# Optimization experiments

Hardware: AMD Instinct MI355X
Metric: run time of the kernel (lower is better)

## Reference

```python
import jax, jax.numpy as jnp
import numpy as np

WIN = (2, 7, 7)
DIL = (1, 2, 2)
SHIFT = (1, 3, 3)
HEADS = 3

def _rel_index(win):
    # relative position index, identical to the torch buffer construction
    cs = np.stack(np.meshgrid(np.arange(win[0]), np.arange(win[1]), np.arange(win[2]), indexing='ij'))
    flat = cs.reshape(3, -1)                                  # (3, N)
    rel = (flat[:, :, None] - flat[:, None, :]).transpose(1, 2, 0)  # (N, N, 3)
    rel[..., 0] += win[0] - 1
    rel[..., 1] += win[1] - 1
    rel[..., 2] += win[2] - 1
    rel[..., 1] *= 2 * win[2] - 1
    rel[..., 0] *= (2 * win[1] - 1) * (2 * win[2] - 1)
    return rel.sum(-1)                                        # (N, N) int

REL_IDX = _rel_index(WIN)

def _partition(x, win, dil):
    # x: (B, S, H, W, C) -> (numWin*B, N, C) with dilated window layout
    B, S, H, W, C = x.shape
    x = x.reshape(B, S // (dil[0] * win[0]), dil[0], win[0],
                  H // (dil[1] * win[1]), dil[1], win[1],
                  W // (dil[2] * win[2]), dil[2], win[2], C)
    x = x.transpose(0, 2, 5, 8, 1, 4, 7, 3, 6, 9, 10)
    return x.reshape(-1, win[0] * win[1] * win[2], C)

def _reverse(wins, win, dil, S, H, W, C):
    B = wins.shape[0] * win[0] * win[1] * win[2] // (S * H * W)
    x = wins.reshape(B, dil[0], dil[1], dil[2],
                     S // (dil[0] * win[0]), H // (dil[1] * win[1]), W // (dil[2] * win[2]),
                     win[0], win[1], win[2], C)
    x = x.transpose(0, 4, 1, 7, 5, 2, 8, 6, 3, 9, 10)
    return x.reshape(B, S, H, W, C)

def setup_inputs() -> dict:
    key = jax.random.key(0)
    ks = jax.random.split(key, 4)
    B, S, H, W, C = 4, 8, 112, 112, 96
    tbl = (2 * WIN[0] - 1) * (2 * WIN[1] - 1) * (2 * WIN[2] - 1)
    return {
        'x': jax.random.normal(ks[0], (B, S * H * W, C), jnp.float32),
        'qkv_w': jax.random.normal(ks[1], (3 * C, C), jnp.float32) * 0.02,
        'qkv_b': jnp.zeros((3 * C,), jnp.float32),
        'proj_w': jax.random.normal(ks[2], (C, C), jnp.float32) * 0.02,
        'proj_b': jnp.zeros((C,), jnp.float32),
        'rel_bias_table': jax.random.normal(ks[3], (tbl, HEADS), jnp.float32) * 0.02,
        'S': 8, 'H': 112, 'W': 112,
    }

def reference(x, qkv_w, qkv_b, proj_w, proj_b, rel_bias_table, S, H, W):
    B, L, C = x.shape
    hd = C // HEADS
    scale = hd ** -0.5
    x = x.reshape(B, S, H, W, C)
    true = tuple(w * d for w, d in zip(WIN, DIL))
    tshift = tuple(s * d for s, d in zip(SHIFT, DIL))
    pad_d = (-S) % true[0]; pad_b = (-H) % true[1]; pad_r = (-W) % true[2]
    x = jnp.pad(x, ((0, 0), (0, pad_d), (0, pad_b), (0, pad_r), (0, 0)))
    Sp, Hp, Wp = S + pad_d, H + pad_b, W + pad_r
    if any(s > 0 for s in SHIFT):
        x = jnp.roll(x, (-tshift[0], -tshift[1], -tshift[2]), axis=(1, 2, 3))
    xw = _partition(x, WIN, DIL)                              # (B_, N, C)
    B_, N, _ = xw.shape
    qkv = (xw @ qkv_w.T + qkv_b).reshape(B_, N, 3, HEADS, hd).transpose(2, 0, 3, 1, 4)
    q, k, v = qkv[0] * scale, qkv[1], qkv[2]                  # (B_, h, N, d)
    attn = jnp.einsum('bhnd,bhmd->bhnm', q, k)
    bias = rel_bias_table[REL_IDX.reshape(-1)].reshape(N, N, HEADS).transpose(2, 0, 1)
    attn = jax.nn.softmax(attn + bias[None], axis=-1)
    out = jnp.einsum('bhnm,bhmd->bhnd', attn, v).transpose(0, 2, 1, 3).reshape(B_, N, C)
    out = out @ proj_w.T + proj_b
    x = _reverse(out, WIN, DIL, Sp, Hp, Wp, C)
    if any(s > 0 for s in SHIFT):
        x = jnp.roll(x, tshift, axis=(1, 2, 3))
    x = x[:, :S, :H, :W, :]
    return x.reshape(B, S * H * W, C)
```

## Files before the change

kernel.cpp:

```cpp
#include <hip/hip_runtime.h>
#include <hip/hip_bf16.h>


typedef __attribute__((ext_vector_type(8))) short short8;
typedef __attribute__((ext_vector_type(4))) float f32x4;

#define WQ_ELEMS (288 * 96)
#define WP_ELEMS (96 * 96)
#define BIAS_ELEMS (3 * 112 * 112)
#define LOG2E 1.4426950408889634f

__device__ __forceinline__ unsigned short f2bf(float f) {
  __hip_bfloat16 h = __float2bfloat16(f);
  return *reinterpret_cast<unsigned short*>(&h);
}

__device__ __forceinline__ unsigned int pack_bf2(float a, float b) {
  unsigned int r;
  asm("v_cvt_pk_bf16_f32 %0, %1, %2" : "=v"(r) : "v"(a), "v"(b));
  return r;
}

__global__ __launch_bounds__(256) void prep_kernel(
    const float* __restrict__ qkv_w, const float* __restrict__ proj_w,
    const float* __restrict__ tbl, unsigned short* __restrict__ wq,
    unsigned short* __restrict__ wp, float* __restrict__ bias) {
  int i = blockIdx.x * 256 + threadIdx.x;
  if (i < WQ_ELEMS) wq[i] = f2bf(qkv_w[i]);
  if (i < WP_ELEMS) wp[i] = f2bf(proj_w[i]);
  if (i < BIAS_ELEMS) {
    int h = i / 12544; int rem = i - h * 12544;
    int m = rem / 112; int n = rem - m * 112;
    float v = -1e30f;
    if (m < 98 && n < 98) {
      int m0 = m / 49, mr = m - m0 * 49, m1 = mr / 7, m2 = mr - m1 * 7;
      int n0 = n / 49, nr = n - n0 * 49, n1 = nr / 7, n2 = nr - n1 * 7;
      int idx = (m0 - n0 + 1) * 169 + (m1 - n1 + 6) * 13 + (m2 - n2 + 6);
      v = tbl[idx * 3 + h] * LOG2E;
    }
    bias[i] = v;
  }
}


__global__ __launch_bounds__(256) void winattn_kernel(
    const float* __restrict__ x, const float* __restrict__ qkv_b,
    const float* __restrict__ proj_b, const unsigned short* __restrict__ wq,
    const unsigned short* __restrict__ wp, const float* __restrict__ bias,
    float* __restrict__ out) {

  __shared__ __align__(16) unsigned short lds[40512];
  __shared__ int eoff[98];

  unsigned short* Qf  = lds;
  unsigned short* Kf  = lds + 9408;
  unsigned short* Vtf = lds + 18816;
  unsigned short* Xf  = lds + 31104;

  const int tid  = threadIdx.x;
  const int wv   = tid >> 6;
  const int lane = tid & 63;
  const int l    = lane & 15;
  const int q    = lane >> 4;

  const short8 zero8 = {0, 0, 0, 0, 0, 0, 0, 0};

  int t1 = blockIdx.x;
  const int wb = t1 & 7;  t1 >>= 3;
  const int hb = t1 & 7;  t1 >>= 3;
  const int sb = t1 & 3;  t1 >>= 2;
  const int d2 = t1 & 1;  t1 >>= 1;
  const int d1 = t1 & 1;  t1 >>= 1;
  const int b  = t1;

  for (int i = tid; i < 768; i += 256)
    reinterpret_cast<unsigned*>(Vtf + 10752)[i] = 0;
  if (tid < 98) {
    int wi0 = tid / 49; int r = tid - wi0 * 49;
    int wi1 = r / 7;    int wi2 = r - wi1 * 7;
    int s  = sb * 2 + wi0;            int so = (s + 1) & 7;
    int hh = (hb * 2 + d1) * 7 + wi1; int ho = hh + 6; if (ho >= 112) ho -= 112;
    int ww = (wb * 2 + d2) * 7 + wi2; int wo = ww + 6; if (wo >= 112) wo -= 112;
    eoff[tid] = (b * 100352 + (so * 112 + ho) * 112 + wo) * 96;
  }
  __syncthreads();

  for (int i = tid; i < 2352; i += 256) {
    int row = i / 24, c4 = i - row * 24;
    float4 v = *reinterpret_cast<const float4*>(x + eoff[row] + c4 * 4);
    uint2 u;
    u.x = pack_bf2(v.x, v.y); u.y = pack_bf2(v.z, v.w);
    *reinterpret_cast<uint2*>(&Xf[((c4 >> 1) * 98 + row) * 8 + (c4 & 1) * 4]) = u;
  }
  __syncthreads();

  const float qscale = 0.17677669529663687f * LOG2E;
  for (int ct = wv; ct < 12; ct += 4) {
    int mch = ct * 16 + l;
    short8 a0 = *reinterpret_cast<const short8*>(wq + mch * 96 +      q * 8);
    short8 a1 = *reinterpret_cast<const short8*>(wq + mch * 96 + 32 + q * 8);
    short8 a2 = *reinterpret_cast<const short8*>(wq + mch * 96 + 64 + q * 8);
    float4 bv = *reinterpret_cast<const float4*>(qkv_b + ct * 16 + q * 4);
    bool isQ = (ct < 6);
    float sc = isQ ? qscale : 1.0f;
    unsigned short* dst = isQ ? Qf : Kf;
    int c0 = (isQ ? ct * 16 : (ct - 6) * 16) + q * 4;
    unsigned short* const dstp = &dst[(c0 >> 3) * 784 + (c0 & 7)];
#pragma unroll
    for (int tt = 0; tt < 7; tt++) {
      int tok = tt * 16 + l;
      short8 b0 = zero8, b1 = zero8, b2 = zero8;
      if (tok < 98) {
        b0 = *reinterpret_cast<const short8*>(&Xf[(( q    ) * 98 + tok) * 8]);
        b1 = *reinterpret_cast<const short8*>(&Xf[((4 + q ) * 98 + tok) * 8]);
        b2 = *reinterpret_cast<const short8*>(&Xf[((8 + q ) * 98 + tok) * 8]);
      }
      f32x4 acc = {0.f, 0.f, 0.f, 0.f};
      acc = __builtin_amdgcn_mfma_f32_16x16x32_bf16(a0, b0, acc, 0, 0, 0);
      acc = __builtin_amdgcn_mfma_f32_16x16x32_bf16(a1, b1, acc, 0, 0, 0);
      acc = __builtin_amdgcn_mfma_f32_16x16x32_bf16(a2, b2, acc, 0, 0, 0);
      uint2 pk;
      pk.x = pack_bf2((acc[0] + bv.x) * sc, (acc[1] + bv.y) * sc);
      pk.y = pack_bf2((acc[2] + bv.z) * sc, (acc[3] + bv.w) * sc);
      if (tok < 98)
        *reinterpret_cast<uint2*>(&dstp[tok * 8]) = pk;
    }
  }

  for (int mt = wv; mt < 7; mt += 4) {
    int tokf = mt * 16 + l;
    short8 a0 = zero8, a1 = zero8, a2 = zero8;
    if (tokf < 98) {
      a0 = *reinterpret_cast<const short8*>(&Xf[(( q    ) * 98 + tokf) * 8]);
      a1 = *reinterpret_cast<const short8*>(&Xf[((4 + q ) * 98 + tokf) * 8]);
      a2 = *reinterpret_cast<const short8*>(&Xf[((8 + q ) * 98 + tokf) * 8]);
    }
    int tok0 = mt * 16 + q * 4;
#pragma unroll
    for (int vt = 0; vt < 6; vt++) {
      int ch = vt * 16 + l;
      short8 b0 = *reinterpret_cast<const short8*>(wq + (192 + ch) * 96 +      q * 8);
      short8 b1 = *reinterpret_cast<const short8*>(wq + (192 + ch) * 96 + 32 + q * 8);
      short8 b2 = *reinterpret_cast<const short8*>(wq + (192 + ch) * 96 + 64 + q * 8);
      f32x4 acc = {0.f, 0.f, 0.f, 0.f};
      acc = __builtin_amdgcn_mfma_f32_16x16x32_bf16(a0, b0, acc, 0, 0, 0);
      acc = __builtin_amdgcn_mfma_f32_16x16x32_bf16(a1, b1, acc, 0, 0, 0);
      acc = __builtin_amdgcn_mfma_f32_16x16x32_bf16(a2, b2, acc, 0, 0, 0);
      float bvv = qkv_b[192 + ch];
      uint2 pk;
      pk.x = pack_bf2(acc[0] + bvv, acc[1] + bvv);
      pk.y = pack_bf2(acc[2] + bvv, acc[3] + bvv);
      *reinterpret_cast<uint2*>(&Vtf[((tok0 >> 3) * 96 + ch) * 8 + (tok0 & 7)]) = pk;
    }
  }
  __syncthreads();

  unsigned short* PwW = Xf + wv * 2048;
  const int pbase = ((q >> 1) * 16 + l) * 8 + (q & 1) * 4;
  const int rbase = (q * 16 + l) * 8;
  {
    uint2 z; z.x = 0; z.y = 0;
    *reinterpret_cast<uint2*>(&PwW[1792 + lane * 4]) = z;
  }
  for (int p = wv; p < 21; p += 4) {
    int h = p / 7, mt = p - h * 7;
    int qtok = mt * 16 + l;
    short8 qa = zero8;
    if (qtok < 98)
      qa = *reinterpret_cast<const short8*>(&Qf[((h * 4 + q) * 98 + qtok) * 8]);
    f32x4 s[7];
#pragma unroll
    for (int nt = 0; nt < 7; nt++) {
      int key = nt * 16 + l;
      short8 kb = zero8;
      if (key < 98)
        kb = *reinterpret_cast<const short8*>(&Kf[((h * 4 + q) * 98 + key) * 8]);
      f32x4 z = {0.f, 0.f, 0.f, 0.f};
      s[nt] = __builtin_amdgcn_mfma_f32_16x16x32_bf16(kb, qa, z, 0, 0, 0);
    }
    const float* bh = bias + h * 12544 + qtok * 112 + q * 4;
#pragma unroll
    for (int nt = 0; nt < 7; nt++) {
      float4 bv = *reinterpret_cast<const float4*>(bh + nt * 16);
      s[nt][0] += bv.x; s[nt][1] += bv.y; s[nt][2] += bv.z; s[nt][3] += bv.w;
    }
    float m[7];
#pragma unroll
    for (int nt = 0; nt < 7; nt++)
      m[nt] = fmaxf(fmaxf(s[nt][0], s[nt][1]), fmaxf(s[nt][2], s[nt][3]));
    float mx = fmaxf(fmaxf(fmaxf(m[0], m[1]), fmaxf(m[2], m[3])),
                     fmaxf(fmaxf(m[4], m[5]), m[6]));
    mx = fmaxf(mx, __shfl_xor(mx, 16));
    mx = fmaxf(mx, __shfl_xor(mx, 32));
    float t[7];
#pragma unroll
    for (int nt = 0; nt < 7; nt++) {
      float e0 = exp2f(s[nt][0] - mx);
      float e1 = exp2f(s[nt][1] - mx);
      float e2 = exp2f(s[nt][2] - mx);
      float e3 = exp2f(s[nt][3] - mx);
      s[nt][0] = e0; s[nt][1] = e1; s[nt][2] = e2; s[nt][3] = e3;
      t[nt] = (e0 + e1) + (e2 + e3);
    }
    float sum = ((t[0] + t[1]) + (t[2] + t[3])) + ((t[4] + t[5]) + t[6]);
    sum += __shfl_xor(sum, 16);
    sum += __shfl_xor(sum, 32);
    float inv = __builtin_amdgcn_rcpf(sum);
#pragma unroll
    for (int nt = 0; nt < 7; nt++) {
      uint2 pk;
      pk.x = pack_bf2(s[nt][0], s[nt][1]);
      pk.y = pack_bf2(s[nt][2], s[nt][3]);
      *reinterpret_cast<uint2*>(&PwW[pbase + nt * 256]) = pk;
    }
    asm volatile("s_waitcnt lgkmcnt(0)" ::: "memory");
    f32x4 o0 = {0.f, 0.f, 0.f, 0.f}, o1 = {0.f, 0.f, 0.f, 0.f};
#pragma unroll
    for (int kt = 0; kt < 4; kt++) {
      short8 pa = *reinterpret_cast<const short8*>(&PwW[rbase + kt * 512]);
      short8 v0 = *reinterpret_cast<const short8*>(&Vtf[((kt * 4 + q) * 96 + h * 32 + l) * 8]);
      short8 v1 = *reinterpret_cast<const short8*>(&Vtf[((kt * 4 + q) * 96 + h * 32 + 16 + l) * 8]);
      o0 = __builtin_amdgcn_mfma_f32_16x16x32_bf16(v0, pa, o0, 0, 0, 0);
      o1 = __builtin_amdgcn_mfma_f32_16x16x32_bf16(v1, pa, o1, 0, 0, 0);
    }
    if (qtok < 98) {
      int c0 = h * 32 + q * 4;
      uint2 pk0;
      pk0.x = pack_bf2(o0[0] * inv, o0[1] * inv);
      pk0.y = pack_bf2(o0[2] * inv, o0[3] * inv);
      *reinterpret_cast<uint2*>(&Qf[((c0 >> 3) * 98 + qtok) * 8 + (c0 & 7)]) = pk0;
      int c1 = c0 + 16;
      uint2 pk1;
      pk1.x = pack_bf2(o1[0] * inv, o1[1] * inv);
      pk1.y = pack_bf2(o1[2] * inv, o1[3] * inv);
      *reinterpret_cast<uint2*>(&Qf[((c1 >> 3) * 98 + qtok) * 8 + (c1 & 7)]) = pk1;
    }
  }
  __syncthreads();

  for (int tt = wv; tt < 7; tt += 4) {
    int tok = tt * 16 + l;
    short8 b0 = zero8, b1 = zero8, b2 = zero8;
    if (tok < 98) {
      b0 = *reinterpret_cast<const short8*>(&Qf[(( q    ) * 98 + tok) * 8]);
      b1 = *reinterpret_cast<const short8*>(&Qf[((4 + q ) * 98 + tok) * 8]);
      b2 = *reinterpret_cast<const short8*>(&Qf[((8 + q ) * 98 + tok) * 8]);
    }
    int off = eoff[(tok < 98) ? tok : 0];
#pragma unroll
    for (int ct = 0; ct < 6; ct++) {
      int mch = ct * 16 + l;
      short8 a0 = *reinterpret_cast<const short8*>(wp + mch * 96 +      q * 8);
      short8 a1 = *reinterpret_cast<const short8*>(wp + mch * 96 + 32 + q * 8);
      short8 a2 = *reinterpret_cast<const short8*>(wp + mch * 96 + 64 + q * 8);
      f32x4 acc = {0.f, 0.f, 0.f, 0.f};
      acc = __builtin_amdgcn_mfma_f32_16x16x32_bf16(a0, b0, acc, 0, 0, 0);
      acc = __builtin_amdgcn_mfma_f32_16x16x32_bf16(a1, b1, acc, 0, 0, 0);
      acc = __builtin_amdgcn_mfma_f32_16x16x32_bf16(a2, b2, acc, 0, 0, 0);
      float4 pb = *reinterpret_cast<const float4*>(proj_b + ct * 16 + q * 4);
      if (tok < 98) {
        float4 o;
        o.x = acc[0] + pb.x; o.y = acc[1] + pb.y;
        o.z = acc[2] + pb.z; o.w = acc[3] + pb.w;
        *reinterpret_cast<float4*>(out + off + ct * 16 + q * 4) = o;
      }
    }
  }
}

extern "C" void kernel_launch(void* const* d_in, const int* in_sizes, int n_in,
                              void* d_out, int out_size, void* d_ws, size_t ws_size,
                              hipStream_t stream) {
  const float* x      = (const float*)d_in[0];
  const float* qkv_w  = (const float*)d_in[1];
  const float* qkv_b  = (const float*)d_in[2];
  const float* proj_w = (const float*)d_in[3];
  const float* proj_b = (const float*)d_in[4];
  const float* tbl    = (const float*)d_in[5];

  unsigned short* wq = (unsigned short*)d_ws;
  unsigned short* wp = wq + WQ_ELEMS;
  float* bias = (float*)((char*)d_ws + (WQ_ELEMS + WP_ELEMS) * 2);

  prep_kernel<<<(BIAS_ELEMS + 255) / 256, 256, 0, stream>>>(qkv_w, proj_w, tbl,
                                                            wq, wp, bias);
  winattn_kernel<<<4096, 256, 0, stream>>>(x, qkv_b, proj_b, wq, wp, bias,
                                           (float*)d_out);
}
```

Measured before the change: 458.4 us.

## Software-pipeline attention tiles with double-buffered scores and hardware exp

Splits the per-tile attention into stages (QK MFMA with bias prefetch, softmax, P store, PV MFMA) and interleaves consecutive tiles in a double-buffered, manually unrolled schedule. Global bias loads and QK MFMAs for the next tile can then overlap the softmax and PV of the current one. Also replaces exp2f with the raw v_exp_f32 instruction and removes an explicit LDS wait. In exchange, register pressure roughly doubles for the score buffers, which may cut occupancy or cause spills.

```diff
diff --git a/kernel.cpp b/kernel.cpp
--- a/kernel.cpp
+++ b/kernel.cpp
@@ -18,6 +18,12 @@
 __device__ __forceinline__ unsigned int pack_bf2(float a, float b) {
   unsigned int r;
   asm("v_cvt_pk_bf16_f32 %0, %1, %2" : "=v"(r) : "v"(a), "v"(b));
+  return r;
+}
+
+__device__ __forceinline__ float exp2_hw(float x) {
+  float r;
+  asm("v_exp_f32 %0, %1" : "=v"(r) : "v"(x));
   return r;
 }
 
@@ -162,13 +168,17 @@
     uint2 z; z.x = 0; z.y = 0;
     *reinterpret_cast<uint2*>(&PwW[1792 + lane * 4]) = z;
   }
-  for (int p = wv; p < 21; p += 4) {
-    int h = p / 7, mt = p - h * 7;
-    int qtok = mt * 16 + l;
+
+  auto Af = [&](int p, f32x4* s, float4* bvv, int& qtok, int& h) {
+    h = p / 7; int mt = p - h * 7;
+    qtok = mt * 16 + l;
+    const float* bh = bias + h * 12544 + qtok * 112 + q * 4;
+#pragma unroll
+    for (int nt = 0; nt < 7; nt++)
+      bvv[nt] = *reinterpret_cast<const float4*>(bh + nt * 16);
     short8 qa = zero8;
     if (qtok < 98)
       qa = *reinterpret_cast<const short8*>(&Qf[((h * 4 + q) * 98 + qtok) * 8]);
-    f32x4 s[7];
 #pragma unroll
     for (int nt = 0; nt < 7; nt++) {
       int key = nt * 16 + l;
@@ -178,42 +188,47 @@
       f32x4 z = {0.f, 0.f, 0.f, 0.f};
       s[nt] = __builtin_amdgcn_mfma_f32_16x16x32_bf16(kb, qa, z, 0, 0, 0);
     }
-    const float* bh = bias + h * 12544 + qtok * 112 + q * 4;
+  };
+
+  auto Bf = [&](f32x4* s, const float4* bvv, uint2* pk, float& inv) {
 #pragma unroll
     for (int nt = 0; nt < 7; nt++) {
-      float4 bv = *reinterpret_cast<const float4*>(bh + nt * 16);
-      s[nt][0] += bv.x; s[nt][1] += bv.y; s[nt][2] += bv.z; s[nt][3] += bv.w;
+      s[nt][0] += bvv[nt].x; s[nt][1] += bvv[nt].y;
+      s[nt][2] += bvv[nt].z; s[nt][3] += bvv[nt].w;
     }
     float m[7];
 #pragma unroll
     for (int nt = 0; nt < 7; nt++)
       m[nt] = fmaxf(fmaxf(s[nt][0], s[nt][1]), fmaxf(s[nt][2], s[nt][3]));
-    float mx = fmaxf(fmaxf(fmaxf(m[0], m[1]), fmaxf(m[2], m[3])),
-                     fmaxf(fmaxf(m[4], m[5]), m[6]));
+    float ma = fmaxf(fmaxf(m[0], m[1]), m[2]);
+    float mb = fmaxf(fmaxf(m[3], m[4]), m[5]);
+    float mx = fmaxf(fmaxf(ma, mb), m[6]);
     mx = fmaxf(mx, __shfl_xor(mx, 16));
     mx = fmaxf(mx, __shfl_xor(mx, 32));
     float t[7];
 #pragma unroll
     for (int nt = 0; nt < 7; nt++) {
-      float e0 = exp2f(s[nt][0] - mx);
-      float e1 = exp2f(s[nt][1] - mx);
-      float e2 = exp2f(s[nt][2] - mx);
-      float e3 = exp2f(s[nt][3] - mx);
-      s[nt][0] = e0; s[nt][1] = e1; s[nt][2] = e2; s[nt][3] = e3;
+      float e0 = exp2_hw(s[nt][0] - mx);
+      float e1 = exp2_hw(s[nt][1] - mx);
+      float e2 = exp2_hw(s[nt][2] - mx);
+      float e3 = exp2_hw(s[nt][3] - mx);
       t[nt] = (e0 + e1) + (e2 + e3);
+      pk[nt].x = pack_bf2(e0, e1);
+      pk[nt].y = pack_bf2(e2, e3);
     }
     float sum = ((t[0] + t[1]) + (t[2] + t[3])) + ((t[4] + t[5]) + t[6]);
     sum += __shfl_xor(sum, 16);
     sum += __shfl_xor(sum, 32);
-    float inv = __builtin_amdgcn_rcpf(sum);
-#pragma unroll
-    for (int nt = 0; nt < 7; nt++) {
-      uint2 pk;
-      pk.x = pack_bf2(s[nt][0], s[nt][1]);
-      pk.y = pack_bf2(s[nt][2], s[nt][3]);
-      *reinterpret_cast<uint2*>(&PwW[pbase + nt * 256]) = pk;
-    }
-    asm volatile("s_waitcnt lgkmcnt(0)" ::: "memory");
+    inv = __builtin_amdgcn_rcpf(sum);
+  };
+
+  auto Cf = [&](const uint2* pk) {
+#pragma unroll
+    for (int nt = 0; nt < 7; nt++)
+      *reinterpret_cast<uint2*>(&PwW[pbase + nt * 256]) = pk[nt];
+  };
+
+  auto DEf = [&](int h, int qtok, float inv) {
     f32x4 o0 = {0.f, 0.f, 0.f, 0.f}, o1 = {0.f, 0.f, 0.f, 0.f};
 #pragma unroll
     for (int kt = 0; kt < 4; kt++) {
@@ -235,6 +250,44 @@
       pk1.y = pack_bf2(o1[2] * inv, o1[3] * inv);
       *reinterpret_cast<uint2*>(&Qf[((c1 >> 3) * 98 + qtok) * 8 + (c1 & 7)]) = pk1;
     }
+  };
+
+  f32x4 sA[7], sB[7];
+  float4 bvA[7], bvB[7];
+  uint2 pkA[7], pkB[7];
+  float ivA, ivB;
+  int hA, hB, qtA, qtB;
+
+  Af(wv, sA, bvA, qtA, hA);
+  Bf(sA, bvA, pkA, ivA);
+
+  Cf(pkA);
+  Af(wv + 4, sB, bvB, qtB, hB);
+  DEf(hA, qtA, ivA);
+  Bf(sB, bvB, pkB, ivB);
+
+  Cf(pkB);
+  Af(wv + 8, sA, bvA, qtA, hA);
+  DEf(hB, qtB, ivB);
+  Bf(sA, bvA, pkA, ivA);
+
+  Cf(pkA);
+  Af(wv + 12, sB, bvB, qtB, hB);
+  DEf(hA, qtA, ivA);
+  Bf(sB, bvB, pkB, ivB);
+
+  Cf(pkB);
+  Af(wv + 16, sA, bvA, qtA, hA);
+  DEf(hB, qtB, ivB);
+  Bf(sA, bvA, pkA, ivA);
+
+  Cf(pkA);
+  if (wv == 0) Af(20, sB, bvB, qtB, hB);
+  DEf(hA, qtA, ivA);
+  if (wv == 0) {
+    Bf(sB, bvB, pkB, ivB);
+    Cf(pkB);
+    DEf(hB, qtB, ivB);
   }
   __syncthreads();
 
```

Measured after the change: 442.2 us. 1.04x faster.

## Double block to 512 threads and rebalance per-window work across eight waves

Applied to the files above, without the earlier changes.

Launches 512-thread blocks (8 waves) per window and redistributes the QKV, attention, and projection work across them. Q/K and V projection tiles now share one loop, and the output projection is split into 42 independent tiles. To fit eight waves in the shared scratch, each wave's P buffer is halved and the PV product is done in two passes. The bias is preloaded as the MFMA accumulator, and exp2 uses the raw v_exp_f32 instruction. This trades more waves per window, and so more latency hiding, for tighter LDS reuse, which needs an added zero-write, and slightly lower exp accuracy.

```diff
diff --git a/kernel.cpp b/kernel.cpp
--- a/kernel.cpp
+++ b/kernel.cpp
@@ -18,6 +18,12 @@
 __device__ __forceinline__ unsigned int pack_bf2(float a, float b) {
   unsigned int r;
   asm("v_cvt_pk_bf16_f32 %0, %1, %2" : "=v"(r) : "v"(a), "v"(b));
+  return r;
+}
+
+__device__ __forceinline__ float exp2_hw(float x) {
+  float r;
+  asm("v_exp_f32 %0, %1" : "=v"(r) : "v"(x));
   return r;
 }
 
@@ -43,7 +49,7 @@
 }
 
 
-__global__ __launch_bounds__(256) void winattn_kernel(
+__global__ __launch_bounds__(512, 4) void winattn_kernel(
     const float* __restrict__ x, const float* __restrict__ qkv_b,
     const float* __restrict__ proj_b, const unsigned short* __restrict__ wq,
     const unsigned short* __restrict__ wp, const float* __restrict__ bias,
@@ -73,7 +79,7 @@
   const int d1 = t1 & 1;  t1 >>= 1;
   const int b  = t1;
 
-  for (int i = tid; i < 768; i += 256)
+  for (int i = tid; i < 768; i += 512)
     reinterpret_cast<unsigned*>(Vtf + 10752)[i] = 0;
   if (tid < 98) {
     int wi0 = tid / 49; int r = tid - wi0 * 49;
@@ -85,7 +91,7 @@
   }
   __syncthreads();
 
-  for (int i = tid; i < 2352; i += 256) {
+  for (int i = tid; i < 2352; i += 512) {
     int row = i / 24, c4 = i - row * 24;
     float4 v = *reinterpret_cast<const float4*>(x + eoff[row] + c4 * 4);
     uint2 u;
@@ -95,129 +101,142 @@
   __syncthreads();
 
   const float qscale = 0.17677669529663687f * LOG2E;
-  for (int ct = wv; ct < 12; ct += 4) {
-    int mch = ct * 16 + l;
-    short8 a0 = *reinterpret_cast<const short8*>(wq + mch * 96 +      q * 8);
-    short8 a1 = *reinterpret_cast<const short8*>(wq + mch * 96 + 32 + q * 8);
-    short8 a2 = *reinterpret_cast<const short8*>(wq + mch * 96 + 64 + q * 8);
-    float4 bv = *reinterpret_cast<const float4*>(qkv_b + ct * 16 + q * 4);
-    bool isQ = (ct < 6);
-    float sc = isQ ? qscale : 1.0f;
-    unsigned short* dst = isQ ? Qf : Kf;
-    int c0 = (isQ ? ct * 16 : (ct - 6) * 16) + q * 4;
-    unsigned short* const dstp = &dst[(c0 >> 3) * 784 + (c0 & 7)];
-#pragma unroll
-    for (int tt = 0; tt < 7; tt++) {
-      int tok = tt * 16 + l;
-      short8 b0 = zero8, b1 = zero8, b2 = zero8;
-      if (tok < 98) {
-        b0 = *reinterpret_cast<const short8*>(&Xf[(( q    ) * 98 + tok) * 8]);
-        b1 = *reinterpret_cast<const short8*>(&Xf[((4 + q ) * 98 + tok) * 8]);
-        b2 = *reinterpret_cast<const short8*>(&Xf[((8 + q ) * 98 + tok) * 8]);
+  for (int j = wv; j < 19; j += 8) {
+    if (j < 12) {
+      int ct = j;
+      int mch = ct * 16 + l;
+      short8 a0 = *reinterpret_cast<const short8*>(wq + mch * 96 +      q * 8);
+      short8 a1 = *reinterpret_cast<const short8*>(wq + mch * 96 + 32 + q * 8);
+      short8 a2 = *reinterpret_cast<const short8*>(wq + mch * 96 + 64 + q * 8);
+      float4 bv = *reinterpret_cast<const float4*>(qkv_b + ct * 16 + q * 4);
+      bool isQ = (ct < 6);
+      float sc = isQ ? qscale : 1.0f;
+      unsigned short* dst = isQ ? Qf : Kf;
+      int c0 = (isQ ? ct * 16 : (ct - 6) * 16) + q * 4;
+      unsigned short* const dstp = &dst[(c0 >> 3) * 784 + (c0 & 7)];
+#pragma unroll
+      for (int tt = 0; tt < 7; tt++) {
+        int tok = tt * 16 + l;
+        short8 b0 = zero8, b1 = zero8, b2 = zero8;
+        if (tok < 98) {
+          b0 = *reinterpret_cast<const short8*>(&Xf[(( q    ) * 98 + tok) * 8]);
+          b1 = *reinterpret_cast<const short8*>(&Xf[((4 + q ) * 98 + tok) * 8]);
+          b2 = *reinterpret_cast<const short8*>(&Xf[((8 + q ) * 98 + tok) * 8]);
+        }
+        f32x4 acc = {0.f, 0.f, 0.f, 0.f};
+        acc = __builtin_amdgcn_mfma_f32_16x16x32_bf16(a0, b0, acc, 0, 0, 0);
+        acc = __builtin_amdgcn_mfma_f32_16x16x32_bf16(a1, b1, acc, 0, 0, 0);
+        acc = __builtin_amdgcn_mfma_f32_16x16x32_bf16(a2, b2, acc, 0, 0, 0);
+        uint2 pk;
+        pk.x = pack_bf2((acc[0] + bv.x) * sc, (acc[1] + bv.y) * sc);
+        pk.y = pack_bf2((acc[2] + bv.z) * sc, (acc[3] + bv.w) * sc);
+        if (tok < 98)
+          *reinterpret_cast<uint2*>(&dstp[tok * 8]) = pk;
       }
-      f32x4 acc = {0.f, 0.f, 0.f, 0.f};
-      acc = __builtin_amdgcn_mfma_f32_16x16x32_bf16(a0, b0, acc, 0, 0, 0);
-      acc = __builtin_amdgcn_mfma_f32_16x16x32_bf16(a1, b1, acc, 0, 0, 0);
-      acc = __builtin_amdgcn_mfma_f32_16x16x32_bf16(a2, b2, acc, 0, 0, 0);
-      uint2 pk;
-      pk.x = pack_bf2((acc[0] + bv.x) * sc, (acc[1] + bv.y) * sc);
-      pk.y = pack_bf2((acc[2] + bv.z) * sc, (acc[3] + bv.w) * sc);
-      if (tok < 98)
-        *reinterpret_cast<uint2*>(&dstp[tok * 8]) = pk;
-    }
-  }
-
-  for (int mt = wv; mt < 7; mt += 4) {
-    int tokf = mt * 16 + l;
-    short8 a0 = zero8, a1 = zero8, a2 = zero8;
-    if (tokf < 98) {
-      a0 = *reinterpret_cast<const short8*>(&Xf[(( q    ) * 98 + tokf) * 8]);
-      a1 = *reinterpret_cast<const short8*>(&Xf[((4 + q ) * 98 + tokf) * 8]);
-      a2 = *reinterpret_cast<const short8*>(&Xf[((8 + q ) * 98 + tokf) * 8]);
-    }
-    int tok0 = mt * 16 + q * 4;
-#pragma unroll
-    for (int vt = 0; vt < 6; vt++) {
-      int ch = vt * 16 + l;
-      short8 b0 = *reinterpret_cast<const short8*>(wq + (192 + ch) * 96 +      q * 8);
-      short8 b1 = *reinterpret_cast<const short8*>(wq + (192 + ch) * 96 + 32 + q * 8);
-      short8 b2 = *reinterpret_cast<const short8*>(wq + (192 + ch) * 96 + 64 + q * 8);
-      f32x4 acc = {0.f, 0.f, 0.f, 0.f};
-      acc = __builtin_amdgcn_mfma_f32_16x16x32_bf16(a0, b0, acc, 0, 0, 0);
-      acc = __builtin_amdgcn_mfma_f32_16x16x32_bf16(a1, b1, acc, 0, 0, 0);
-      acc = __builtin_amdgcn_mfma_f32_16x16x32_bf16(a2, b2, acc, 0, 0, 0);
-      float bvv = qkv_b[192 + ch];
-      uint2 pk;
-      pk.x = pack_bf2(acc[0] + bvv, acc[1] + bvv);
-      pk.y = pack_bf2(acc[2] + bvv, acc[3] + bvv);
-      *reinterpret_cast<uint2*>(&Vtf[((tok0 >> 3) * 96 + ch) * 8 + (tok0 & 7)]) = pk;
+    } else {
+      int mt = j - 12;
+      int tokf = mt * 16 + l;
+      short8 a0 = zero8, a1 = zero8, a2 = zero8;
+      if (tokf < 98) {
+        a0 = *reinterpret_cast<const short8*>(&Xf[(( q    ) * 98 + tokf) * 8]);
+        a1 = *reinterpret_cast<const short8*>(&Xf[((4 + q ) * 98 + tokf) * 8]);
+        a2 = *reinterpret_cast<const short8*>(&Xf[((8 + q ) * 98 + tokf) * 8]);
+      }
+      int tok0 = mt * 16 + q * 4;
+#pragma unroll
+      for (int vt = 0; vt < 6; vt++) {
+        int ch = vt * 16 + l;
+        short8 b0 = *reinterpret_cast<const short8*>(wq + (192 + ch) * 96 +      q * 8);
+        short8 b1 = *reinterpret_cast<const short8*>(wq + (192 + ch) * 96 + 32 + q * 8);
+        short8 b2 = *reinterpret_cast<const short8*>(wq + (192 + ch) * 96 + 64 + q * 8);
+        f32x4 acc = {0.f, 0.f, 0.f, 0.f};
+        acc = __builtin_amdgcn_mfma_f32_16x16x32_bf16(a0, b0, acc, 0, 0, 0);
+        acc = __builtin_amdgcn_mfma_f32_16x16x32_bf16(a1, b1, acc, 0, 0, 0);
+        acc = __builtin_amdgcn_mfma_f32_16x16x32_bf16(a2, b2, acc, 0, 0, 0);
+        float bvv = qkv_b[192 + ch];
+        uint2 pk;
+        pk.x = pack_bf2(acc[0] + bvv, acc[1] + bvv);
+        pk.y = pack_bf2(acc[2] + bvv, acc[3] + bvv);
+        *reinterpret_cast<uint2*>(&Vtf[((tok0 >> 3) * 96 + ch) * 8 + (tok0 & 7)]) = pk;
+      }
     }
   }
   __syncthreads();
 
-  unsigned short* PwW = Xf + wv * 2048;
+  unsigned short* PwW = Xf + wv * 1024;
   const int pbase = ((q >> 1) * 16 + l) * 8 + (q & 1) * 4;
   const int rbase = (q * 16 + l) * 8;
-  {
-    uint2 z; z.x = 0; z.y = 0;
-    *reinterpret_cast<uint2*>(&PwW[1792 + lane * 4]) = z;
-  }
-  for (int p = wv; p < 21; p += 4) {
+
+  for (int p = wv; p < 21; p += 8) {
     int h = p / 7, mt = p - h * 7;
     int qtok = mt * 16 + l;
+    const float* bh = bias + h * 12544 + qtok * 112 + q * 4;
+    f32x4 s[7];
+#pragma unroll
+    for (int nt = 0; nt < 7; nt++) {
+      float4 bv = *reinterpret_cast<const float4*>(bh + nt * 16);
+      f32x4 a = {bv.x, bv.y, bv.z, bv.w};
+      s[nt] = a;
+    }
     short8 qa = zero8;
     if (qtok < 98)
       qa = *reinterpret_cast<const short8*>(&Qf[((h * 4 + q) * 98 + qtok) * 8]);
-    f32x4 s[7];
 #pragma unroll
     for (int nt = 0; nt < 7; nt++) {
       int key = nt * 16 + l;
       short8 kb = zero8;
       if (key < 98)
         kb = *reinterpret_cast<const short8*>(&Kf[((h * 4 + q) * 98 + key) * 8]);
-      f32x4 z = {0.f, 0.f, 0.f, 0.f};
-      s[nt] = __builtin_amdgcn_mfma_f32_16x16x32_bf16(kb, qa, z, 0, 0, 0);
-    }
-    const float* bh = bias + h * 12544 + qtok * 112 + q * 4;
-#pragma unroll
-    for (int nt = 0; nt < 7; nt++) {
-      float4 bv = *reinterpret_cast<const float4*>(bh + nt * 16);
-      s[nt][0] += bv.x; s[nt][1] += bv.y; s[nt][2] += bv.z; s[nt][3] += bv.w;
+      s[nt] = __builtin_amdgcn_mfma_f32_16x16x32_bf16(kb, qa, s[nt], 0, 0, 0);
     }
     float m[7];
 #pragma unroll
     for (int nt = 0; nt < 7; nt++)
       m[nt] = fmaxf(fmaxf(s[nt][0], s[nt][1]), fmaxf(s[nt][2], s[nt][3]));
-    float mx = fmaxf(fmaxf(fmaxf(m[0], m[1]), fmaxf(m[2], m[3])),
-                     fmaxf(fmaxf(m[4], m[5]), m[6]));
+    float ma = fmaxf(fmaxf(m[0], m[1]), m[2]);
+    float mb = fmaxf(fmaxf(m[3], m[4]), m[5]);
+    float mx = fmaxf(fmaxf(ma, mb), m[6]);
     mx = fmaxf(mx, __shfl_xor(mx, 16));
     mx = fmaxf(mx, __shfl_xor(mx, 32));
     float t[7];
+    uint2 pk[7];
 #pragma unroll
     for (int nt = 0; nt < 7; nt++) {
-      float e0 = exp2f(s[nt][0] - mx);
-      float e1 = exp2f(s[nt][1] - mx);
-      float e2 = exp2f(s[nt][2] - mx);
-      float e3 = exp2f(s[nt][3] - mx);
-      s[nt][0] = e0; s[nt][1] = e1; s[nt][2] = e2; s[nt][3] = e3;
+      float e0 = exp2_hw(s[nt][0] - mx);
+      float e1 = exp2_hw(s[nt][1] - mx);
+      float e2 = exp2_hw(s[nt][2] - mx);
+      float e3 = exp2_hw(s[nt][3] - mx);
       t[nt] = (e0 + e1) + (e2 + e3);
+      pk[nt].x = pack_bf2(e0, e1);
+      pk[nt].y = pack_bf2(e2, e3);
     }
     float sum = ((t[0] + t[1]) + (t[2] + t[3])) + ((t[4] + t[5]) + t[6]);
     sum += __shfl_xor(sum, 16);
     sum += __shfl_xor(sum, 32);
     float inv = __builtin_amdgcn_rcpf(sum);
-#pragma unroll
-    for (int nt = 0; nt < 7; nt++) {
-      uint2 pk;
-      pk.x = pack_bf2(s[nt][0], s[nt][1]);
-      pk.y = pack_bf2(s[nt][2], s[nt][3]);
-      *reinterpret_cast<uint2*>(&PwW[pbase + nt * 256]) = pk;
-    }
-    asm volatile("s_waitcnt lgkmcnt(0)" ::: "memory");
+
     f32x4 o0 = {0.f, 0.f, 0.f, 0.f}, o1 = {0.f, 0.f, 0.f, 0.f};
 #pragma unroll
-    for (int kt = 0; kt < 4; kt++) {
+    for (int nt = 0; nt < 4; nt++)
+      *reinterpret_cast<uint2*>(&PwW[pbase + nt * 256]) = pk[nt];
+#pragma unroll
+    for (int kt = 0; kt < 2; kt++) {
       short8 pa = *reinterpret_cast<const short8*>(&PwW[rbase + kt * 512]);
+      short8 v0 = *reinterpret_cast<const short8*>(&Vtf[((kt * 4 + q) * 96 + h * 32 + l) * 8]);
+      short8 v1 = *reinterpret_cast<const short8*>(&Vtf[((kt * 4 + q) * 96 + h * 32 + 16 + l) * 8]);
+      o0 = __builtin_amdgcn_mfma_f32_16x16x32_bf16(v0, pa, o0, 0, 0, 0);
+      o1 = __builtin_amdgcn_mfma_f32_16x16x32_bf16(v1, pa, o1, 0, 0, 0);
+    }
+    {
+      uint2 z; z.x = 0; z.y = 0;
+      *reinterpret_cast<uint2*>(&PwW[768 + lane * 4]) = z;
+    }
+#pragma unroll
+    for (int nt = 4; nt < 7; nt++)
+      *reinterpret_cast<uint2*>(&PwW[pbase + (nt - 4) * 256]) = pk[nt];
+#pragma unroll
+    for (int kt = 2; kt < 4; kt++) {
+      short8 pa = *reinterpret_cast<const short8*>(&PwW[rbase + (kt - 2) * 512]);
       short8 v0 = *reinterpret_cast<const short8*>(&Vtf[((kt * 4 + q) * 96 + h * 32 + l) * 8]);
       short8 v1 = *reinterpret_cast<const short8*>(&Vtf[((kt * 4 + q) * 96 + h * 32 + 16 + l) * 8]);
       o0 = __builtin_amdgcn_mfma_f32_16x16x32_bf16(v0, pa, o0, 0, 0, 0);
@@ -238,7 +257,12 @@
   }
   __syncthreads();
 
-  for (int tt = wv; tt < 7; tt += 4) {
+  for (int t = wv; t < 42; t += 8) {
+    int ct = t / 7, tt = t - ct * 7;
+    int mch = ct * 16 + l;
+    short8 a0 = *reinterpret_cast<const short8*>(wp + mch * 96 +      q * 8);
+    short8 a1 = *reinterpret_cast<const short8*>(wp + mch * 96 + 32 + q * 8);
+    short8 a2 = *reinterpret_cast<const short8*>(wp + mch * 96 + 64 + q * 8);
     int tok = tt * 16 + l;
     short8 b0 = zero8, b1 = zero8, b2 = zero8;
     if (tok < 98) {
@@ -246,24 +270,16 @@
       b1 = *reinterpret_cast<const short8*>(&Qf[((4 + q ) * 98 + tok) * 8]);
       b2 = *reinterpret_cast<const short8*>(&Qf[((8 + q ) * 98 + tok) * 8]);
     }
-    int off = eoff[(tok < 98) ? tok : 0];
-#pragma unroll
-    for (int ct = 0; ct < 6; ct++) {
-      int mch = ct * 16 + l;
-      short8 a0 = *reinterpret_cast<const short8*>(wp + mch * 96 +      q * 8);
-      short8 a1 = *reinterpret_cast<const short8*>(wp + mch * 96 + 32 + q * 8);
-      short8 a2 = *reinterpret_cast<const short8*>(wp + mch * 96 + 64 + q * 8);
-      f32x4 acc = {0.f, 0.f, 0.f, 0.f};
-      acc = __builtin_amdgcn_mfma_f32_16x16x32_bf16(a0, b0, acc, 0, 0, 0);
-      acc = __builtin_amdgcn_mfma_f32_16x16x32_bf16(a1, b1, acc, 0, 0, 0);
-      acc = __builtin_amdgcn_mfma_f32_16x16x32_bf16(a2, b2, acc, 0, 0, 0);
-      float4 pb = *reinterpret_cast<const float4*>(proj_b + ct * 16 + q * 4);
-      if (tok < 98) {
-        float4 o;
-        o.x = acc[0] + pb.x; o.y = acc[1] + pb.y;
-        o.z = acc[2] + pb.z; o.w = acc[3] + pb.w;
-        *reinterpret_cast<float4*>(out + off + ct * 16 + q * 4) = o;
-      }
+    f32x4 acc = {0.f, 0.f, 0.f, 0.f};
+    acc = __builtin_amdgcn_mfma_f32_16x16x32_bf16(a0, b0, acc, 0, 0, 0);
+    acc = __builtin_amdgcn_mfma_f32_16x16x32_bf16(a1, b1, acc, 0, 0, 0);
+    acc = __builtin_amdgcn_mfma_f32_16x16x32_bf16(a2, b2, acc, 0, 0, 0);
+    float4 pb = *reinterpret_cast<const float4*>(proj_b + ct * 16 + q * 4);
+    if (tok < 98) {
+      float4 o;
+      o.x = acc[0] + pb.x; o.y = acc[1] + pb.y;
+      o.z = acc[2] + pb.z; o.w = acc[3] + pb.w;
+      *reinterpret_cast<float4*>(out + eoff[tok] + ct * 16 + q * 4) = o;
     }
   }
 }
@@ -284,6 +300,6 @@
 
   prep_kernel<<<(BIAS_ELEMS + 255) / 256, 256, 0, stream>>>(qkv_w, proj_w, tbl,
                                                             wq, wp, bias);
-  winattn_kernel<<<4096, 256, 0, stream>>>(x, qkv_b, proj_b, wq, wp, bias,
+  winattn_kernel<<<4096, 512, 0, stream>>>(x, qkv_b, proj_b, wq, wp, bias,
                                            (float*)d_out);
 }
```

After: 399.0 us. 13.0% less time.
